# Performance work log

Hardware: AMD Instinct MI355X
Metric: run time of the kernel (lower is better)

Reference implementation:

```python
import jax, jax.numpy as jnp
import numpy as np

N = 40000      # nodes
E = 320000     # edges (avg degree 8)
F = 512        # feats_in_size
H = 256        # num_hidden_nodes
HEADS = 8      # num_attention_heads
NEG_SLOPE = 0.01  # torch LeakyReLU default


def setup_inputs() -> dict:
    key = jax.random.key(0)
    k = jax.random.split(key, 8)
    feats = jax.random.normal(k[0], (N, F), jnp.float32)
    # strictly upper-triangular edges (dst > src) so the original module's
    # in-place sequential update equals the parallel segment-softmax GAT
    src = jax.random.randint(k[1], (E,), 0, N - 1, dtype=jnp.int32)
    dst = src + jax.random.randint(k[2], (E,), 1, N - src, dtype=jnp.int32)
    adj_ind = jnp.stack([src, dst], axis=0)  # [2, E]
    adjacency_matrix = jnp.zeros((1, 1), jnp.float32)  # unused when adj_ind given
    W_w = jax.random.normal(k[3], (F, H), jnp.float32) * 0.05   # Linear weight (transposed)
    W_b = jax.random.normal(k[4], (H,), jnp.float32) * 0.05
    attn_w = jax.random.normal(k[5], (HEADS, 2 * H), jnp.float32) * 0.05  # per-head [1,2H] stacked
    attn_b = jax.random.normal(k[6], (HEADS,), jnp.float32) * 0.05
    return {"feats": feats, "adjacency_matrix": adjacency_matrix, "adj_ind": adj_ind,
            "W_w": W_w, "W_b": W_b, "attn_w": attn_w, "attn_b": attn_b}


def reference(feats, adjacency_matrix, adj_ind, W_w, W_b, attn_w, attn_b):
    src, dst = adj_ind[0], adj_ind[1]
    h = feats @ W_w + W_b                       # [N, H]
    h_src = h[src]                              # [E, H] gather
    h_dst = h[dst]                              # [E, H] gather
    # attn_i(cat(h_src, h_dst)) == h_src @ a_i[:H] + h_dst @ a_i[H:] + b_i
    a_s, a_d = attn_w[:, :H], attn_w[:, H:]     # [HEADS, H] each
    scores = h_src @ a_s.T + h_dst @ a_d.T + attn_b  # [E, HEADS]
    scores = jax.nn.leaky_relu(scores, NEG_SLOPE)
    # segment softmax over outgoing edges of each src node
    m = jax.ops.segment_max(scores, src, num_segments=N)   # [N, HEADS]
    ex = jnp.exp(scores - m[src])
    denom = jax.ops.segment_sum(ex, src, num_segments=N)   # [N, HEADS]
    alpha = ex / denom[src]                                 # [E, HEADS]
    # per-head: out_i[u] = h[u] + sum_{(u,v)} alpha_i(u,v) * h[v]
    outs = [h + jax.ops.segment_sum(alpha[:, i:i + 1] * h_dst, src, num_segments=N)
            for i in range(HEADS)]
    return jnp.concatenate(outs, axis=1)        # [N, HEADS*H]
```

## Files before the change

kernel.cpp:

```cpp
#include <hip/hip_runtime.h>

typedef __attribute__((ext_vector_type(8))) short short8v;
typedef __attribute__((ext_vector_type(4))) float f32x4;

#define NN 40000
#define FF 512
#define HH 256
#define EE 320000
#define NHEADS 8
#define NEG_SLOPE 0.01f
#define NB 157

__device__ __forceinline__ short f2bf(float x) {
    unsigned u = __float_as_uint(x);
    u += 0x7fffu + ((u >> 16) & 1u);
    return (short)(u >> 16);
}
__device__ __forceinline__ float bf2f(unsigned short b) {
    return __uint_as_float(((unsigned)b) << 16);
}

__global__ void prep_kernel(const float* __restrict__ W, short* __restrict__ Wt,
                            const int* __restrict__ src, int* __restrict__ deg) {
    int b = blockIdx.x;
    if (b < 512) {
        int i = b * 256 + threadIdx.x;
        int k = i >> 8, n = i & 255;
        Wt[n * 512 + k] = f2bf(W[i]);
    } else {
        int e = (b - 512) * 256 + threadIdx.x;
        if (e < EE) atomicAdd(&deg[src[e]], 1);
    }
}

__global__ __launch_bounds__(512) void gemm_kernel(
    const float* __restrict__ feats,
    const short* __restrict__ Btf,
    const float* __restrict__ bias,
    unsigned short* __restrict__ h2)
{
    __shared__ short8v ldsA[512];
    __shared__ short8v ldsB[2048];
    const int tid = threadIdx.x;
    const int lane = tid & 63, w = tid >> 6;
    const int wm = w >> 2, wn = w & 3;
    const int r0 = blockIdx.x * 64;

    const int arow = tid >> 3, aslot = tid & 7;

    float4 regA[2];
    short8v regB[4];

    auto stage_loadA = [&](int k0) {
        const float* p = feats + (size_t)(r0 + arow) * 512 + k0 + aslot * 8;
        regA[0] = *reinterpret_cast<const float4*>(p);
        regA[1] = *reinterpret_cast<const float4*>(p + 4);
    };
    auto stage_loadB = [&](int k0) {
        #pragma unroll
        for (int c = 0; c < 4; ++c) {
            int u = tid + c * 512;
            int row = u >> 3, slot = u & 7;
            regB[c] = *reinterpret_cast<const short8v*>(Btf + (size_t)row * 512 + k0 + slot * 8);
        }
    };
    auto stage_store = [&]() {
        short8v v;
        #pragma unroll
        for (int j = 0; j < 4; ++j) {
            v[j]     = f2bf(regA[0][j]);
            v[4 + j] = f2bf(regA[1][j]);
        }
        ldsA[arow * 8 + (aslot ^ (arow & 7))] = v;
        #pragma unroll
        for (int c = 0; c < 4; ++c) {
            int u = tid + c * 512;
            int row = u >> 3, slot = u & 7;
            ldsB[row * 8 + (slot ^ (row & 7))] = regB[c];
        }
    };

    f32x4 acc[2][4];
    #pragma unroll
    for (int i = 0; i < 2; ++i)
        #pragma unroll
        for (int j = 0; j < 4; ++j)
            acc[i][j] = {0.f, 0.f, 0.f, 0.f};

    stage_loadA(0);
    stage_loadB(0);

    for (int kt = 0; kt < 8; ++kt) {
        __syncthreads();
        stage_store();
        __syncthreads();
        if (kt < 7) {
            stage_loadA((kt + 1) * 64);
            stage_loadB((kt + 1) * 64);
        }
        #pragma unroll
        for (int kc = 0; kc < 2; ++kc) {
            short8v af[2], bfr[4];
            int kslot = kc * 4 + (lane >> 4);
            #pragma unroll
            for (int mr = 0; mr < 2; ++mr) {
                int row = wm * 32 + mr * 16 + (lane & 15);
                af[mr] = ldsA[row * 8 + (kslot ^ (row & 7))];
            }
            #pragma unroll
            for (int nr = 0; nr < 4; ++nr) {
                int col = wn * 64 + nr * 16 + (lane & 15);
                bfr[nr] = ldsB[col * 8 + (kslot ^ (col & 7))];
            }
            #pragma unroll
            for (int mr = 0; mr < 2; ++mr)
                #pragma unroll
                for (int nr = 0; nr < 4; ++nr)
                    acc[mr][nr] = __builtin_amdgcn_mfma_f32_16x16x32_bf16(
                        af[mr], bfr[nr], acc[mr][nr], 0, 0, 0);
        }
    }

    #pragma unroll
    for (int mr = 0; mr < 2; ++mr) {
        #pragma unroll
        for (int nr = 0; nr < 4; ++nr) {
            int gc = wn * 64 + nr * 16 + (lane & 15);
            float b = bias[gc];
            #pragma unroll
            for (int j = 0; j < 4; ++j) {
                int gr = r0 + wm * 32 + mr * 16 + (lane >> 4) * 4 + j;
                h2[(size_t)gr * 256 + gc] = (unsigned short)f2bf(acc[mr][nr][j] + b);
            }
        }
    }
}

__global__ __launch_bounds__(256) void sproj_kernel(
    const unsigned short* __restrict__ h2, const float* __restrict__ attn_w,
    float* __restrict__ s_src, float* __restrict__ s_dst)
{
    int wid = threadIdx.x >> 6, lane = threadIdx.x & 63;
    int n = blockIdx.x * 4 + wid;
    if (n >= NN) return;
    ushort4 hb = *reinterpret_cast<const ushort4*>(h2 + (size_t)n * 256 + lane * 4);
    float4 hv = {bf2f(hb.x), bf2f(hb.y), bf2f(hb.z), bf2f(hb.w)};

    float ss[8], sd[8];
    #pragma unroll
    for (int q = 0; q < 8; ++q) {
        float4 as = *reinterpret_cast<const float4*>(attn_w + q * 512 + lane * 4);
        float4 ad = *reinterpret_cast<const float4*>(attn_w + q * 512 + 256 + lane * 4);
        ss[q] = hv.x * as.x + hv.y * as.y + hv.z * as.z + hv.w * as.w;
        sd[q] = hv.x * ad.x + hv.y * ad.y + hv.z * ad.z + hv.w * ad.w;
    }
    #pragma unroll
    for (int q = 0; q < 8; ++q) {
        #pragma unroll
        for (int off = 32; off >= 1; off >>= 1) {
            ss[q] += __shfl_xor(ss[q], off);
            sd[q] += __shfl_xor(sd[q], off);
        }
    }
    if (lane == 0) {
        #pragma unroll
        for (int q = 0; q < 8; ++q) {
            s_src[(size_t)n * 8 + q] = ss[q];
            s_dst[(size_t)n * 8 + q] = sd[q];
        }
    }
}

__global__ __launch_bounds__(256) void scan1_kernel(const int* __restrict__ deg,
                                                    int* __restrict__ rowtmp,
                                                    int* __restrict__ partials)
{
    __shared__ int buf[256];
    int tid = threadIdx.x;
    int i = blockIdx.x * 256 + tid;
    int v = (i < NN) ? deg[i] : 0;
    buf[tid] = v;
    __syncthreads();
    #pragma unroll
    for (int off = 1; off < 256; off <<= 1) {
        int t = (tid >= off) ? buf[tid - off] : 0;
        __syncthreads();
        buf[tid] += t;
        __syncthreads();
    }
    if (i < NN) rowtmp[i] = buf[tid] - v;
    if (tid == 255) partials[blockIdx.x] = buf[255];
}

__global__ __launch_bounds__(256) void scan23_kernel(const int* __restrict__ rowtmp,
                                                     const int* __restrict__ partials,
                                                     int* __restrict__ rowstart)
{
    __shared__ int buf[256];
    __shared__ int offs[256];
    int tid = threadIdx.x;
    int v = (tid < NB) ? partials[tid] : 0;
    buf[tid] = v;
    __syncthreads();
    #pragma unroll
    for (int off = 1; off < 256; off <<= 1) {
        int t = (tid >= off) ? buf[tid - off] : 0;
        __syncthreads();
        buf[tid] += t;
        __syncthreads();
    }
    offs[tid] = buf[tid] - v;
    __syncthreads();
    int myoff = offs[blockIdx.x];
    int i = blockIdx.x * 256 + tid;
    if (i < NN) rowstart[i] = rowtmp[i] + myoff;
    if (blockIdx.x == 0 && tid == 0) rowstart[NN] = EE;
}

__global__ void edgefill_kernel(const int* __restrict__ src, const int* __restrict__ dst,
                                const float* __restrict__ s_src, const float* __restrict__ s_dst,
                                const float* __restrict__ attn_b,
                                const int* __restrict__ rowstart, int* __restrict__ cursor,
                                int* __restrict__ csrDst, float* __restrict__ exSlot)
{
    int e = blockIdx.x * 256 + threadIdx.x;
    if (e >= EE) return;
    int s = src[e], d = dst[e];
    float4 a0 = reinterpret_cast<const float4*>(s_src + (size_t)s * 8)[0];
    float4 a1 = reinterpret_cast<const float4*>(s_src + (size_t)s * 8)[1];
    float4 c0 = reinterpret_cast<const float4*>(s_dst + (size_t)d * 8)[0];
    float4 c1 = reinterpret_cast<const float4*>(s_dst + (size_t)d * 8)[1];
    float4 b0 = reinterpret_cast<const float4*>(attn_b)[0];
    float4 b1 = reinterpret_cast<const float4*>(attn_b)[1];
    float v[8];
    v[0] = a0.x + c0.x + b0.x; v[1] = a0.y + c0.y + b0.y;
    v[2] = a0.z + c0.z + b0.z; v[3] = a0.w + c0.w + b0.w;
    v[4] = a1.x + c1.x + b1.x; v[5] = a1.y + c1.y + b1.y;
    v[6] = a1.z + c1.z + b1.z; v[7] = a1.w + c1.w + b1.w;
    #pragma unroll
    for (int q = 0; q < 8; ++q) {
        float sc = v[q] > 0.f ? v[q] : NEG_SLOPE * v[q];
        v[q] = __expf(sc);
    }
    int pos = atomicAdd(&cursor[s], 1);
    int slot = rowstart[s] + pos;
    csrDst[slot] = d;
    float4 o0 = {v[0], v[1], v[2], v[3]};
    float4 o1 = {v[4], v[5], v[6], v[7]};
    reinterpret_cast<float4*>(exSlot + (size_t)slot * 8)[0] = o0;
    reinterpret_cast<float4*>(exSlot + (size_t)slot * 8)[1] = o1;
}

__global__ __launch_bounds__(256) void agg_kernel(
    const unsigned short* __restrict__ h2,
    const float* __restrict__ exSlot,
    const int* __restrict__ csrDst, const int* __restrict__ rowstart,
    float* __restrict__ out)
{
    int wid = threadIdx.x >> 6, lane = threadIdx.x & 63;
    int n = blockIdx.x * 4 + wid;
    if (n >= NN) return;
    int start = rowstart[n];
    int deg = rowstart[n + 1] - start;
    int ei = lane >> 3;

    ushort4 sb = *reinterpret_cast<const ushort4*>(h2 + (size_t)n * 256 + lane * 4);
    f32x4 hv = {bf2f(sb.x), bf2f(sb.y), bf2f(sb.z), bf2f(sb.w)};
    f32x4 acc[8];
    #pragma unroll
    for (int q = 0; q < 8; ++q) acc[q] = {0.f, 0.f, 0.f, 0.f};
    float den = 0.f;

    for (int base = 0; base < deg; base += 8) {
        int idx = base + ei;
        int dd = 0;
        if (idx < deg) dd = csrDst[start + idx];
        float ex = 0.f;
        int lpos = base * 8 + lane;
        if (lpos < deg * 8) ex = exSlot[(size_t)start * 8 + lpos];
        den += ex;
        int cnt = min(8, deg - base);
        for (int t = 0; t < cnt; ++t) {
            int ddt = __shfl(dd, t * 8);
            ushort4 hb = *reinterpret_cast<const ushort4*>(h2 + (size_t)ddt * 256 + lane * 4);
            f32x4 hd = {bf2f(hb.x), bf2f(hb.y), bf2f(hb.z), bf2f(hb.w)};
            #pragma unroll
            for (int q = 0; q < 8; ++q) {
                float exq = __shfl(ex, t * 8 + q);
                acc[q] += hd * exq;
            }
        }
    }

    den += __shfl_xor(den, 8);
    den += __shfl_xor(den, 16);
    den += __shfl_xor(den, 32);

    float* orow = out + (size_t)n * 2048;
    #pragma unroll
    for (int q = 0; q < 8; ++q) {
        float dq = __shfl(den, q);
        float r = dq > 0.f ? 1.f / dq : 0.f;
        f32x4 o = hv + acc[q] * r;
        *reinterpret_cast<f32x4*>(orow + q * 256 + lane * 4) = o;
    }
}

extern "C" void kernel_launch(void* const* d_in, const int* in_sizes, int n_in,
                              void* d_out, int out_size, void* d_ws, size_t ws_size,
                              hipStream_t stream) {
    const float* feats  = (const float*)d_in[0];
    const int*   adj    = (const int*)d_in[2];
    const float* W_w    = (const float*)d_in[3];
    const float* W_b    = (const float*)d_in[4];
    const float* attn_w = (const float*)d_in[5];
    const float* attn_b = (const float*)d_in[6];
    float* out = (float*)d_out;
    const int* srcA = adj;
    const int* dstA = adj + EE;

    char* ws = (char*)d_ws;
    size_t off = 0;
    auto alloc = [&](size_t bytes) -> void* {
        void* p = ws + off;
        off += (bytes + 255) & ~(size_t)255;
        return p;
    };
    short* Wt            = (short*)alloc((size_t)HH * FF * 2);
    unsigned short* h2   = (unsigned short*)alloc((size_t)NN * HH * 2);
    float* s_src   = (float*)alloc((size_t)NN * 8 * 4);
    float* s_dst   = (float*)alloc((size_t)NN * 8 * 4);
    float* exSlot  = (float*)alloc((size_t)EE * 8 * 4);
    int*   deg     = (int*)alloc((size_t)NN * 4 * 2);
    int*   cursor  = deg + NN;
    int*   rowtmp  = (int*)alloc((size_t)NN * 4);
    int*   partials= (int*)alloc((size_t)256 * 4);
    int*   rowstart= (int*)alloc((size_t)(NN + 1) * 4);
    int*   csrDst  = (int*)alloc((size_t)EE * 4);

    hipMemsetAsync(deg, 0, (size_t)2 * NN * 4, stream);
    prep_kernel<<<512 + (EE + 255) / 256, 256, 0, stream>>>(W_w, Wt, srcA, deg);
    scan1_kernel<<<NB, 256, 0, stream>>>(deg, rowtmp, partials);
    scan23_kernel<<<NB, 256, 0, stream>>>(rowtmp, partials, rowstart);
    gemm_kernel<<<NN / 64, 512, 0, stream>>>(feats, Wt, W_b, h2);
    sproj_kernel<<<NN / 4, 256, 0, stream>>>(h2, attn_w, s_src, s_dst);
    edgefill_kernel<<<(EE + 255) / 256, 256, 0, stream>>>(srcA, dstA, s_src, s_dst, attn_b,
                                                          rowstart, cursor, csrDst, exSlot);
    agg_kernel<<<NN / 4, 256, 0, stream>>>(h2, exSlot, csrDst, rowstart, out);
}
```

Baseline: 214.5 us.

## Compute edge attention scores inside aggregation instead of materializing exSlot

The per-edge score computation (leaky-relu plus exp of s_src+s_dst+bias) moves out of the edge-fill kernel and into the aggregation kernel. Each lane there computes its own head's score from gathered s_dst values. The bias is folded into s_src in the projection kernel. The CSR fill kernel now only scatters destination indices and no longer depends on the GEMM outputs, so it launches before the GEMM. This removes the 10 MB exSlot write and its later read, at the cost of an extra random gather of s_dst per edge in the aggregation.

New measurement: 211.5 us. No clear change (-1.4%).

```diff
diff --git a/kernel.cpp b/kernel.cpp
--- a/kernel.cpp
+++ b/kernel.cpp
@@ -138,6 +138,7 @@
 
 __global__ __launch_bounds__(256) void sproj_kernel(
     const unsigned short* __restrict__ h2, const float* __restrict__ attn_w,
+    const float* __restrict__ attn_b,
     float* __restrict__ s_src, float* __restrict__ s_dst)
 {
     int wid = threadIdx.x >> 6, lane = threadIdx.x & 63;
@@ -165,7 +166,7 @@
     if (lane == 0) {
         #pragma unroll
         for (int q = 0; q < 8; ++q) {
-            s_src[(size_t)n * 8 + q] = ss[q];
+            s_src[(size_t)n * 8 + q] = ss[q] + attn_b[q];
             s_dst[(size_t)n * 8 + q] = sd[q];
         }
     }
@@ -217,43 +218,20 @@
     if (blockIdx.x == 0 && tid == 0) rowstart[NN] = EE;
 }
 
-__global__ void edgefill_kernel(const int* __restrict__ src, const int* __restrict__ dst,
-                                const float* __restrict__ s_src, const float* __restrict__ s_dst,
-                                const float* __restrict__ attn_b,
-                                const int* __restrict__ rowstart, int* __restrict__ cursor,
-                                int* __restrict__ csrDst, float* __restrict__ exSlot)
+__global__ void fill_kernel(const int* __restrict__ src, const int* __restrict__ dst,
+                            const int* __restrict__ rowstart,
+                            int* __restrict__ cursor, int* __restrict__ csrDst)
 {
     int e = blockIdx.x * 256 + threadIdx.x;
     if (e >= EE) return;
-    int s = src[e], d = dst[e];
-    float4 a0 = reinterpret_cast<const float4*>(s_src + (size_t)s * 8)[0];
-    float4 a1 = reinterpret_cast<const float4*>(s_src + (size_t)s * 8)[1];
-    float4 c0 = reinterpret_cast<const float4*>(s_dst + (size_t)d * 8)[0];
-    float4 c1 = reinterpret_cast<const float4*>(s_dst + (size_t)d * 8)[1];
-    float4 b0 = reinterpret_cast<const float4*>(attn_b)[0];
-    float4 b1 = reinterpret_cast<const float4*>(attn_b)[1];
-    float v[8];
-    v[0] = a0.x + c0.x + b0.x; v[1] = a0.y + c0.y + b0.y;
-    v[2] = a0.z + c0.z + b0.z; v[3] = a0.w + c0.w + b0.w;
-    v[4] = a1.x + c1.x + b1.x; v[5] = a1.y + c1.y + b1.y;
-    v[6] = a1.z + c1.z + b1.z; v[7] = a1.w + c1.w + b1.w;
-    #pragma unroll
-    for (int q = 0; q < 8; ++q) {
-        float sc = v[q] > 0.f ? v[q] : NEG_SLOPE * v[q];
-        v[q] = __expf(sc);
-    }
+    int s = src[e];
     int pos = atomicAdd(&cursor[s], 1);
-    int slot = rowstart[s] + pos;
-    csrDst[slot] = d;
-    float4 o0 = {v[0], v[1], v[2], v[3]};
-    float4 o1 = {v[4], v[5], v[6], v[7]};
-    reinterpret_cast<float4*>(exSlot + (size_t)slot * 8)[0] = o0;
-    reinterpret_cast<float4*>(exSlot + (size_t)slot * 8)[1] = o1;
+    csrDst[rowstart[s] + pos] = dst[e];
 }
 
 __global__ __launch_bounds__(256) void agg_kernel(
     const unsigned short* __restrict__ h2,
-    const float* __restrict__ exSlot,
+    const float* __restrict__ s_src, const float* __restrict__ s_dst,
     const int* __restrict__ csrDst, const int* __restrict__ rowstart,
     float* __restrict__ out)
 {
@@ -262,7 +240,9 @@
     if (n >= NN) return;
     int start = rowstart[n];
     int deg = rowstart[n + 1] - start;
-    int ei = lane >> 3;
+    int ei = lane >> 3, hh = lane & 7;
+
+    float ssrc = s_src[(size_t)n * 8 + hh];
 
     ushort4 sb = *reinterpret_cast<const ushort4*>(h2 + (size_t)n * 256 + lane * 4);
     f32x4 hv = {bf2f(sb.x), bf2f(sb.y), bf2f(sb.z), bf2f(sb.w)};
@@ -273,11 +253,14 @@
 
     for (int base = 0; base < deg; base += 8) {
         int idx = base + ei;
-        int dd = 0;
-        if (idx < deg) dd = csrDst[start + idx];
+        int dd = 0; bool valid = idx < deg;
+        if (valid) dd = csrDst[start + idx];
         float ex = 0.f;
-        int lpos = base * 8 + lane;
-        if (lpos < deg * 8) ex = exSlot[(size_t)start * 8 + lpos];
+        if (valid) {
+            float sc = ssrc + s_dst[(size_t)dd * 8 + hh];
+            sc = sc > 0.f ? sc : NEG_SLOPE * sc;
+            ex = __expf(sc);
+        }
         den += ex;
         int cnt = min(8, deg - base);
         for (int t = 0; t < cnt; ++t) {
@@ -330,7 +313,6 @@
     unsigned short* h2   = (unsigned short*)alloc((size_t)NN * HH * 2);
     float* s_src   = (float*)alloc((size_t)NN * 8 * 4);
     float* s_dst   = (float*)alloc((size_t)NN * 8 * 4);
-    float* exSlot  = (float*)alloc((size_t)EE * 8 * 4);
     int*   deg     = (int*)alloc((size_t)NN * 4 * 2);
     int*   cursor  = deg + NN;
     int*   rowtmp  = (int*)alloc((size_t)NN * 4);
@@ -342,9 +324,8 @@
     prep_kernel<<<512 + (EE + 255) / 256, 256, 0, stream>>>(W_w, Wt, srcA, deg);
     scan1_kernel<<<NB, 256, 0, stream>>>(deg, rowtmp, partials);
     scan23_kernel<<<NB, 256, 0, stream>>>(rowtmp, partials, rowstart);
+    fill_kernel<<<(EE + 255) / 256, 256, 0, stream>>>(srcA, dstA, rowstart, cursor, csrDst);
     gemm_kernel<<<NN / 64, 512, 0, stream>>>(feats, Wt, W_b, h2);
-    sproj_kernel<<<NN / 4, 256, 0, stream>>>(h2, attn_w, s_src, s_dst);
-    edgefill_kernel<<<(EE + 255) / 256, 256, 0, stream>>>(srcA, dstA, s_src, s_dst, attn_b,
-                                                          rowstart, cursor, csrDst, exSlot);
-    agg_kernel<<<NN / 4, 256, 0, stream>>>(h2, exSlot, csrDst, rowstart, out);
-}
+    sproj_kernel<<<NN / 4, 256, 0, stream>>>(h2, attn_w, attn_b, s_src, s_dst);
+    agg_kernel<<<NN / 4, 256, 0, stream>>>(h2, s_src, s_dst, csrDst, rowstart, out);
+}
```
